# Kernel tuning notes

Measured on AMD Instinct MI355X. Metric: run time of the kernel, lower is better.

Reference implementation:

```python
import jax, jax.numpy as jnp
import numpy as np

D_MODEL = 1024
NUM_HEADS = 16
HEAD_DIM = D_MODEL // NUM_HEADS  # 64
SCALE = HEAD_DIM ** -0.5
BIAS_LEN = 128  # min(max_seq_len=512, 128)
ROPE_BASE = 10000.0
LN_EPS = 1e-5


def setup_inputs() -> dict:
    key = jax.random.key(0)
    ks = jax.random.split(key, 8)
    B, Lq, Lkv = 8, 512, 512
    return {
        "decoder_hidden": jax.random.normal(ks[0], (B, Lq, D_MODEL), jnp.float32),
        "encoder_output": jax.random.normal(ks[1], (B, Lkv, D_MODEL), jnp.float32),
        "Wqkv": jax.random.normal(ks[2], (3 * D_MODEL, D_MODEL), jnp.float32) * 0.02,
        "Wout": jax.random.normal(ks[3], (D_MODEL, D_MODEL), jnp.float32) * 0.02,
        "b_out": jnp.zeros((D_MODEL,), jnp.float32),
        "Wgate": jax.random.normal(ks[4], (D_MODEL, D_MODEL), jnp.float32) * 0.02,
        "b_gate": jnp.zeros((D_MODEL,), jnp.float32),
        "gamma": jnp.ones((D_MODEL,), jnp.float32),
        "beta": jnp.zeros((D_MODEL,), jnp.float32),
    }


def _layernorm(x, gamma, beta):
    mu = jnp.mean(x, axis=-1, keepdims=True)
    var = jnp.mean(jnp.square(x - mu), axis=-1, keepdims=True)
    return (x - mu) * jax.lax.rsqrt(var + LN_EPS) * gamma + beta


def _rope(x, cos, sin):
    # x: [B, H, L, HEAD_DIM]; cos/sin: [L, HEAD_DIM//2]
    half = HEAD_DIM // 2
    c = cos[None, None, :, :]
    s = sin[None, None, :, :]
    x_even, x_odd = x[..., :half], x[..., half:]
    return jnp.concatenate([x_even * c - x_odd * s, x_even * s + x_odd * c], axis=-1)


def _temporal_bias(L_q, L_kv):
    pos = jnp.arange(BIAS_LEN, dtype=jnp.float32)
    dist = jnp.abs(pos[None, :] - pos[:, None])  # [128,128]
    bias = jnp.exp(-dist * 0.1) - dist * 0.05
    if L_q <= BIAS_LEN and L_kv <= BIAS_LEN:
        return bias[:L_q, :L_kv]
    # bilinear interpolation (align_corners=False / half-pixel) fallback
    return jax.image.resize(bias, (L_q, L_kv), method="bilinear")


def reference(decoder_hidden, encoder_output, Wqkv, Wout, b_out, Wgate, b_gate, gamma, beta):
    B, L_q, _ = decoder_hidden.shape
    L_kv = encoder_output.shape[1]
    residual = decoder_hidden

    q_in = _layernorm(decoder_hidden, gamma, beta)
    kv_in = _layernorm(encoder_output, gamma, beta)

    q = q_in @ Wqkv[:D_MODEL].T
    k = kv_in @ Wqkv[D_MODEL:2 * D_MODEL].T
    v = kv_in @ Wqkv[2 * D_MODEL:].T

    q = q.reshape(B, L_q, NUM_HEADS, HEAD_DIM).transpose(0, 2, 1, 3)
    k = k.reshape(B, L_kv, NUM_HEADS, HEAD_DIM).transpose(0, 2, 1, 3)
    v = v.reshape(B, L_kv, NUM_HEADS, HEAD_DIM).transpose(0, 2, 1, 3)

    # rotary embedding over max(L_q, L_kv) positions
    L = max(L_q, L_kv)
    inv_freq = 1.0 / ROPE_BASE ** (jnp.arange(0, HEAD_DIM, 2, dtype=jnp.float32) / HEAD_DIM)
    freqs = jnp.arange(L, dtype=jnp.float32)[:, None] * inv_freq[None, :]  # [L, HEAD_DIM//2]
    cos, sin = jnp.cos(freqs), jnp.sin(freqs)
    q = _rope(q, cos[:L_q], sin[:L_q])
    k = _rope(k, cos[:L_kv], sin[:L_kv])

    scores = jnp.einsum("bhqd,bhkd->bhqk", q, k) * SCALE
    scores = scores + _temporal_bias(L_q, L_kv)[None, None, :, :]

    attn = jax.nn.softmax(scores, axis=-1)
    attended = jnp.einsum("bhqk,bhkd->bhqd", attn, v)
    attended = attended.transpose(0, 2, 1, 3).reshape(B, L_q, D_MODEL)
    attended = attended @ Wout.T + b_out

    gate = jax.nn.sigmoid(attended @ Wgate.T + b_gate)
    output = gate * attended + (1.0 - gate) * residual
    return output
```

## Files before the change

kernel.cpp:

```cpp
#include <hip/hip_runtime.h>
#include <hip/hip_bf16.h>

#define D_MODEL 1024
#define NHEADS 16
#define HDIM 64
#define BATCH 8
#define SEQ 512
#define NROWS 4096
#define SCALE 0.125f
#define LN_EPS 1e-5f

typedef __attribute__((ext_vector_type(8))) short bf16x8;
typedef __attribute__((ext_vector_type(4))) float f32x4;
typedef __attribute__((ext_vector_type(8))) unsigned short u16x8;

static __device__ __forceinline__ float bf2f(unsigned short u) {
    return __uint_as_float(((unsigned int)u) << 16);
}
static __device__ __forceinline__ unsigned short f2bf(float f) {
    unsigned int x = __float_as_uint(f);
    unsigned int r = (x + 0x7fffu + ((x >> 16) & 1u)) >> 16;
    return (unsigned short)r;
}

#define GLOAD16(gp, lp)                                                        \
    __builtin_amdgcn_global_load_lds(                                          \
        (const __attribute__((address_space(1))) void*)(gp),                   \
        (__attribute__((address_space(3))) void*)(lp), 16, 0, 0)

static __device__ __forceinline__ float bias128(int a, int b) {
    float d = fabsf((float)(a - b));
    return expf(-d * 0.1f) - d * 0.05f;
}

__global__ void prep_kernel(const float* __restrict__ dec, const float* __restrict__ enc,
                            const float* __restrict__ gamma, const float* __restrict__ beta,
                            const float* __restrict__ Wqkv,
                            const float* __restrict__ Wout, const float* __restrict__ Wgate,
                            unsigned short* __restrict__ q_ln, unsigned short* __restrict__ kv_ln,
                            float* __restrict__ bias, unsigned short* __restrict__ Wqkv_bf,
                            unsigned short* __restrict__ Wout_bf, unsigned short* __restrict__ Wgate_bf) {
    int blk = blockIdx.x;
    int t = threadIdx.x;
    if (blk >= 12288) {
        int idx = (blk - 12288) * 256 + t;
        const float* src; unsigned short* dst; int off;
        if (idx < 262144) { src = Wout; dst = Wout_bf; off = idx; }
        else              { src = Wgate; dst = Wgate_bf; off = idx - 262144; }
        float4 v = ((const float4*)src)[off];
        ushort4 u;
        u.x = f2bf(v.x); u.y = f2bf(v.y); u.z = f2bf(v.z); u.w = f2bf(v.w);
        ((ushort4*)dst)[off] = u;
        return;
    }
    if (blk >= 9216) {
        int idx = (blk - 9216) * 256 + t;
        float4 v = ((const float4*)Wqkv)[idx];
        ushort4 u;
        u.x = f2bf(v.x); u.y = f2bf(v.y); u.z = f2bf(v.z); u.w = f2bf(v.w);
        ((ushort4*)Wqkv_bf)[idx] = u;
        return;
    }
    if (blk >= 8192) {
        int idx = (blk - 8192) * 256 + t;
        int qi = idx >> 9, kj = idx & 511;
        float fq = (qi + 0.5f) * 0.25f - 0.5f;
        float fk = (kj + 0.5f) * 0.25f - 0.5f;
        int iq = (int)floorf(fq); float tq = fq - (float)iq;
        int ik = (int)floorf(fk); float tk = fk - (float)ik;
        int iq0 = min(max(iq, 0), 127), iq1 = min(max(iq + 1, 0), 127);
        int ik0 = min(max(ik, 0), 127), ik1 = min(max(ik + 1, 0), 127);
        float v = (1.f - tq) * ((1.f - tk) * bias128(iq0, ik0) + tk * bias128(iq0, ik1))
                +        tq  * ((1.f - tk) * bias128(iq1, ik0) + tk * bias128(iq1, ik1));
        bias[idx] = v;
        return;
    }
    int row = blk;
    const float* src = (row < NROWS) ? dec + (size_t)row * D_MODEL
                                     : enc + (size_t)(row - NROWS) * D_MODEL;
    unsigned short* dst = (row < NROWS) ? q_ln + (size_t)row * D_MODEL
                                        : kv_ln + (size_t)(row - NROWS) * D_MODEL;
    float4 x = ((const float4*)src)[t];
    float s  = x.x + x.y + x.z + x.w;
    float ss = x.x * x.x + x.y * x.y + x.z * x.z + x.w * x.w;
    #pragma unroll
    for (int off = 32; off > 0; off >>= 1) {
        s  += __shfl_down(s, off);
        ss += __shfl_down(ss, off);
    }
    __shared__ float red_s[4], red_ss[4];
    int wid = t >> 6, lane = t & 63;
    if (lane == 0) { red_s[wid] = s; red_ss[wid] = ss; }
    __syncthreads();
    if (t == 0) {
        float S = red_s[0] + red_s[1] + red_s[2] + red_s[3];
        float SS = red_ss[0] + red_ss[1] + red_ss[2] + red_ss[3];
        red_s[0] = S; red_ss[0] = SS;
    }
    __syncthreads();
    float mu  = red_s[0] * (1.0f / 1024.0f);
    float var = red_ss[0] * (1.0f / 1024.0f) - mu * mu;
    float rstd = rsqrtf(var + LN_EPS);
    float4 g = ((const float4*)gamma)[t];
    float4 bb = ((const float4*)beta)[t];
    ushort4 u;
    u.x = f2bf((x.x - mu) * rstd * g.x + bb.x);
    u.y = f2bf((x.y - mu) * rstd * g.y + bb.y);
    u.z = f2bf((x.z - mu) * rstd * g.z + bb.z);
    u.w = f2bf((x.w - mu) * rstd * g.w + bb.w);
    ((ushort4*)dst)[t] = u;
}

__global__ void convert_og(const float* __restrict__ Wout, const float* __restrict__ Wgate,
                           unsigned short* __restrict__ Wout_bf, unsigned short* __restrict__ Wgate_bf) {
    int idx = blockIdx.x * 256 + threadIdx.x;
    const float* src; unsigned short* dst; int off;
    if (idx < 262144) { src = (const float*)Wout; dst = Wout_bf; off = idx; }
    else              { src = (const float*)Wgate; dst = Wgate_bf; off = idx - 262144; }
    float4 v = ((const float4*)src)[off];
    ushort4 u;
    u.x = f2bf(v.x); u.y = f2bf(v.y); u.z = f2bf(v.z); u.w = f2bf(v.w);
    ((ushort4*)dst)[off] = u;
}

#define CSTR 136

struct alignas(16) Smem64B {
    unsigned short A[64 * 128];
    unsigned short B[128 * 128];
};

union alignas(16) Smem64Q {
    struct { unsigned short A[64 * 128]; unsigned short B[128 * 128]; } ab;
    unsigned short C[64 * CSTR];
    unsigned short Ct[128 * 72];
};

#define MF(a, b, d) __builtin_amdgcn_mfma_f32_16x16x32_bf16((a), (b), (d), 0, 0, 0)

#define GEMM_KH2B(kh)                                                          \
    {                                                                          \
        int pofs = (((kh) * 4 + quad) ^ c) * 8;                                \
        const unsigned short* Arow_ = &As2[(wr * 32 + c) * 128 + pofs];        \
        const unsigned short* Brow_ = &Bs2[(wc * 64 + c) * 128 + pofs];        \
        bf16x8 f0 = *(const bf16x8*)(Arow_);                                   \
        bf16x8 f1 = *(const bf16x8*)(Arow_ + 2048);                            \
        bf16x8 g0 = *(const bf16x8*)(Brow_);                                   \
        bf16x8 g1 = *(const bf16x8*)(Brow_ + 2048);                            \
        bf16x8 g2 = *(const bf16x8*)(Brow_ + 4096);                            \
        bf16x8 g3 = *(const bf16x8*)(Brow_ + 6144);                            \
        c00 = MF(f0, g0, c00); c01 = MF(f0, g1, c01); c02 = MF(f0, g2, c02); c03 = MF(f0, g3, c03); \
        c10 = MF(f1, g0, c10); c11 = MF(f1, g1, c11); c12 = MF(f1, g2, c12); c13 = MF(f1, g3, c13); \
    }

#define GEMM_BODY_64B(Aptr, Bptr)                                              \
    int wave = tid >> 6, lane = tid & 63, quad = lane >> 4, c = lane & 15;     \
    int wr = wave >> 1, wc = wave & 1;                                         \
    int l4 = lane >> 4, l15 = lane & 15;                                       \
    const unsigned short* Abase = (Aptr) + (size_t)(rt * 64) * 1024;           \
    const unsigned short* Bbase = (Bptr) + (size_t)(ct * 128) * 1024;          \
    int aoff0 = (wave * 16 +  0 + l4) * 1024 + ((l15 ^ ( 0 + l4)) * 8);        \
    int aoff1 = (wave * 16 +  4 + l4) * 1024 + ((l15 ^ ( 4 + l4)) * 8);        \
    int aoff2 = (wave * 16 +  8 + l4) * 1024 + ((l15 ^ ( 8 + l4)) * 8);        \
    int aoff3 = (wave * 16 + 12 + l4) * 1024 + ((l15 ^ (12 + l4)) * 8);        \
    int boff0 = (wave * 32 +  0 + l4) * 1024 + ((l15 ^ (( 0 + l4) & 15)) * 8); \
    int boff1 = (wave * 32 +  4 + l4) * 1024 + ((l15 ^ (( 4 + l4) & 15)) * 8); \
    int boff2 = (wave * 32 +  8 + l4) * 1024 + ((l15 ^ (( 8 + l4) & 15)) * 8); \
    int boff3 = (wave * 32 + 12 + l4) * 1024 + ((l15 ^ ((12 + l4) & 15)) * 8); \
    int boff4 = (wave * 32 + 16 + l4) * 1024 + ((l15 ^ ((16 + l4) & 15)) * 8); \
    int boff5 = (wave * 32 + 20 + l4) * 1024 + ((l15 ^ ((20 + l4) & 15)) * 8); \
    int boff6 = (wave * 32 + 24 + l4) * 1024 + ((l15 ^ ((24 + l4) & 15)) * 8); \
    int boff7 = (wave * 32 + 28 + l4) * 1024 + ((l15 ^ ((28 + l4) & 15)) * 8); \
    unsigned short* AsW = As2 + wave * 2048;                                   \
    unsigned short* BsW = Bs2 + wave * 4096;                                   \
    f32x4 c00 = (f32x4)0.f, c01 = (f32x4)0.f, c02 = (f32x4)0.f, c03 = (f32x4)0.f; \
    f32x4 c10 = (f32x4)0.f, c11 = (f32x4)0.f, c12 = (f32x4)0.f, c13 = (f32x4)0.f; \
    for (int kt = 0; kt < 8; ++kt) {                                           \
        int k0 = kt * 128;                                                     \
        __syncthreads();                                                       \
        GLOAD16(Abase + aoff0 + k0, AsW);                                      \
        GLOAD16(Abase + aoff1 + k0, AsW + 512);                                \
        GLOAD16(Abase + aoff2 + k0, AsW + 1024);                               \
        GLOAD16(Abase + aoff3 + k0, AsW + 1536);                               \
        GLOAD16(Bbase + boff0 + k0, BsW);                                      \
        GLOAD16(Bbase + boff1 + k0, BsW + 512);                                \
        GLOAD16(Bbase + boff2 + k0, BsW + 1024);                               \
        GLOAD16(Bbase + boff3 + k0, BsW + 1536);                               \
        GLOAD16(Bbase + boff4 + k0, BsW + 2048);                               \
        GLOAD16(Bbase + boff5 + k0, BsW + 2560);                               \
        GLOAD16(Bbase + boff6 + k0, BsW + 3072);                               \
        GLOAD16(Bbase + boff7 + k0, BsW + 3584);                               \
        __syncthreads();                                                       \
        GEMM_KH2B(0)                                                           \
        GEMM_KH2B(1)                                                           \
        GEMM_KH2B(2)                                                           \
        GEMM_KH2B(3)                                                           \
    }

#define QROPE_REG(i, reg, A0, A1, A2, A3)                                      \
    {                                                                          \
        int mloc = wr * 32 + (i) * 16 + quad * 4 + (reg);                      \
        int crow = mloc * CSTR + wc * 64;                                      \
        float fl = (float)((rt * 64 + mloc) & 511);                            \
        float aa0 = fl * inv0, aa1 = fl * inv1;                                \
        float c0 = cosf(aa0), s0 = sinf(aa0);                                  \
        float c1 = cosf(aa1), s1 = sinf(aa1);                                  \
        float e0 = A0[(reg)], o0 = A2[(reg)];                                  \
        float e1 = A1[(reg)], o1 = A3[(reg)];                                  \
        smemq.C[crow + c]      = f2bf(e0 * c0 - o0 * s0);                      \
        smemq.C[crow + 32 + c] = f2bf(e0 * s0 + o0 * c0);                      \
        smemq.C[crow + 16 + c] = f2bf(e1 * c1 - o1 * s1);                      \
        smemq.C[crow + 48 + c] = f2bf(e1 * s1 + o1 * c1);                      \
    }
#define QROPE_ROW(i, A0, A1, A2, A3)                                           \
    QROPE_REG(i, 0, A0, A1, A2, A3) QROPE_REG(i, 1, A0, A1, A2, A3)            \
    QROPE_REG(i, 2, A0, A1, A2, A3) QROPE_REG(i, 3, A0, A1, A2, A3)

#define QVSECT_REG(i, j, reg, Acc)                                             \
    smemq.Ct[(wc * 64 + (j) * 16 + c) * 72 + (wr * 32 + (i) * 16 + quad * 4 + (reg))] = f2bf(Acc[(reg)]);
#define QVSECT_TILE(i, j, Acc)                                                 \
    QVSECT_REG(i, j, 0, Acc) QVSECT_REG(i, j, 1, Acc)                          \
    QVSECT_REG(i, j, 2, Acc) QVSECT_REG(i, j, 3, Acc)

__global__ __launch_bounds__(256, 1)
void qkv_gemm_mfma(const unsigned short* __restrict__ q_ln,
                   const unsigned short* __restrict__ kv_ln,
                   const unsigned short* __restrict__ Wb,
                   unsigned short* __restrict__ qo,
                   unsigned short* __restrict__ ko,
                   unsigned short* __restrict__ vo) {
    int bid = blockIdx.x;
    int st = bid >> 5, in = bid & 31;
    int stc = st % 3, str = st / 3;
    int ct = stc * 8 + (in & 7);
    int rt = str * 4 + (in >> 3);
    int n0 = ct * 128;
    int section = n0 >> 10;
    const unsigned short* A = (section == 0) ? q_ln : kv_ln;

    __shared__ Smem64Q smemq;
    unsigned short* As2 = smemq.ab.A;
    unsigned short* Bs2 = smemq.ab.B;
    int tid = threadIdx.x;

    GEMM_BODY_64B(A, Wb)

    __syncthreads();
    if (section == 2) {
        QVSECT_TILE(0, 0, c00) QVSECT_TILE(0, 1, c01) QVSECT_TILE(0, 2, c02) QVSECT_TILE(0, 3, c03)
        QVSECT_TILE(1, 0, c10) QVSECT_TILE(1, 1, c11) QVSECT_TILE(1, 2, c12) QVSECT_TILE(1, 3, c13)
        __syncthreads();
        int dr = tid >> 1, hh = tid & 1;
        int h = ((n0 & 1023) >> 6) + (dr >> 6);
        int d = dr & 63;
        int mmb = rt * 64;
        int bb = mmb >> 9, ll0 = mmb & 511;
        unsigned short* orow = vo + (((size_t)bb * NHEADS + h) * HDIM + d) * SEQ + ll0 + hh * 32;
        const unsigned short* csrc = &smemq.Ct[dr * 72 + hh * 32];
        #pragma unroll
        for (int kc = 0; kc < 4; ++kc)
            *(u16x8*)(orow + kc * 8) = *(const u16x8*)(csrc + kc * 8);
        return;
    }

    float inv0 = expf(-0.2878231366f * (float)c);
    float inv1 = expf(-0.2878231366f * (float)(16 + c));
    QROPE_ROW(0, c00, c01, c02, c03)
    QROPE_ROW(1, c10, c11, c12, c13)
    __syncthreads();

    unsigned short* outp = (section == 0) ? qo : ko;
    int rr = tid >> 2;
    int ch = (tid >> 1) & 1;
    int sub = tid & 1;
    int mm = rt * 64 + rr;
    int bb = mm >> 9, ll = mm & 511;
    int h = ((n0 & 1023) >> 6) + ch;
    unsigned short* orow = outp + (((size_t)bb * NHEADS + h) * SEQ + ll) * HDIM + sub * 32;
    const unsigned short* csrc = &smemq.C[rr * CSTR + ch * 64 + sub * 32];
    #pragma unroll
    for (int kc = 0; kc < 4; ++kc)
        *(u16x8*)(orow + kc * 8) = *(const u16x8*)(csrc + kc * 8);
}

#define O1_REG(mb, reg, n, Acc)                                                \
    t_bf[(size_t)((mb) + (reg)) * 1024 + (n)] = f2bf(Acc[(reg)] + bo);
#define O1_TILE(i, j, Acc)                                                     \
    {                                                                          \
        int n = ct * 128 + wc * 64 + (j) * 16 + c;                             \
        float bo = b_out[n];                                                   \
        int mb = rt * 64 + wr * 32 + (i) * 16 + quad * 4;                      \
        O1_REG(mb, 0, n, Acc) O1_REG(mb, 1, n, Acc)                            \
        O1_REG(mb, 2, n, Acc) O1_REG(mb, 3, n, Acc)                            \
    }

__global__ __launch_bounds__(256, 1)
void out_gemm1_mfma(const unsigned short* __restrict__ att,
                    const unsigned short* __restrict__ Wob,
                    const float* __restrict__ b_out,
                    unsigned short* __restrict__ t_bf) {
    int ct = blockIdx.x, rt = blockIdx.y;
    __shared__ Smem64B smem2;
    unsigned short* As2 = smem2.A;
    unsigned short* Bs2 = smem2.B;
    int tid = threadIdx.x;

    GEMM_BODY_64B(att, Wob)

    O1_TILE(0, 0, c00) O1_TILE(0, 1, c01) O1_TILE(0, 2, c02) O1_TILE(0, 3, c03)
    O1_TILE(1, 0, c10) O1_TILE(1, 1, c11) O1_TILE(1, 2, c12) O1_TILE(1, 3, c13)
}

#define O2_REG(mb, reg, n, Acc)                                                \
    {                                                                          \
        float gz = Acc[(reg)] + bg;                                            \
        float g = 1.0f / (1.0f + expf(-gz));                                   \
        size_t idx = (size_t)((mb) + (reg)) * 1024 + (n);                      \
        float tv = bf2f(t_bf[idx]);                                            \
        float rv = residual[idx];                                              \
        out[idx] = g * tv + (1.0f - g) * rv;                                   \
    }
#define O2_TILE(i, j, Acc)                                                     \
    {                                                                          \
        int n = ct * 128 + wc * 64 + (j) * 16 + c;                             \
        float bg = b_gate[n];                                                  \
        int mb = rt * 64 + wr * 32 + (i) * 16 + quad * 4;                      \
        O2_REG(mb, 0, n, Acc) O2_REG(mb, 1, n, Acc)                            \
        O2_REG(mb, 2, n, Acc) O2_REG(mb, 3, n, Acc)                            \
    }

__global__ __launch_bounds__(256, 1)
void out_gemm2_mfma(const unsigned short* __restrict__ t_bf,
                    const unsigned short* __restrict__ Wgb,
                    const float* __restrict__ b_gate,
                    const float* __restrict__ residual,
                    float* __restrict__ out) {
    int ct = blockIdx.x, rt = blockIdx.y;
    __shared__ Smem64B smem2;
    unsigned short* As2 = smem2.A;
    unsigned short* Bs2 = smem2.B;
    int tid = threadIdx.x;

    GEMM_BODY_64B(t_bf, Wgb)

    O2_TILE(0, 0, c00) O2_TILE(0, 1, c01) O2_TILE(0, 2, c02) O2_TILE(0, 3, c03)
    O2_TILE(1, 0, c10) O2_TILE(1, 1, c11) O2_TILE(1, 2, c12) O2_TILE(1, 3, c13)
}

#define KSTR 72

__global__ __launch_bounds__(512)
void attn_kernel(const unsigned short* __restrict__ q,
                 const unsigned short* __restrict__ k,
                 const unsigned short* __restrict__ vt,
                 const float* __restrict__ bias,
                 unsigned short* __restrict__ attended) {
    int qt = blockIdx.x, h = blockIdx.y, b = blockIdx.z;
    __shared__ unsigned short Ks[64 * 64];
    __shared__ unsigned short Vs[64 * 64];
    __shared__ unsigned short Ps[128 * KSTR];
    __shared__ float lf[128];

    int tid = threadIdx.x;
    int wave = tid >> 6, lane = tid & 63;
    int quad = lane >> 4, c = lane & 15;
    int wb = wave * 16;
    size_t headbase = (((size_t)b * NHEADS + h) * SEQ) * HDIM;
    int q0 = qt * 128;

    const unsigned short* qrow = q + headbase + (size_t)(q0 + wb + c) * HDIM;
    bf16x8 aq0 = *(const bf16x8*)(qrow + quad * 8);
    bf16x8 aq1 = *(const bf16x8*)(qrow + 32 + quad * 8);

    int srow = wave * 8 + (lane >> 3);
    int schunk = (lane & 7) ^ (srow & 7);
    unsigned short* KsW = Ks + wave * 512;
    unsigned short* VsW = Vs + wave * 512;
    const unsigned short* kgb = k + headbase + (size_t)srow * HDIM + schunk * 8;
    const unsigned short* vgb = vt + headbase + (size_t)srow * SEQ + schunk * 8;
    int x7 = c & 7;
    int p0 = (quad ^ x7) * 8;
    int p1 = ((4 + quad) ^ x7) * 8;

    f32x4 oacc[4];
    #pragma unroll
    for (int t = 0; t < 4; ++t) oacc[t] = (f32x4)0.f;
    float lrow[4];
    #pragma unroll
    for (int r = 0; r < 4; ++r) lrow[r] = 0.f;

    for (int kt = 0; kt < 8; ++kt) {
        int kv0 = kt * 64;
        __syncthreads();
        GLOAD16(kgb + (size_t)kv0 * HDIM, KsW);
        GLOAD16(vgb + kv0, VsW);
        __syncthreads();

        f32x4 sacc[4];
        #pragma unroll
        for (int nt = 0; nt < 4; ++nt) {
            const unsigned short* kbase = &Ks[(nt * 16 + c) * 64];
            bf16x8 b0 = *(const bf16x8*)(kbase + p0);
            bf16x8 b1 = *(const bf16x8*)(kbase + p1);
            f32x4 a = (f32x4)0.f;
            a = __builtin_amdgcn_mfma_f32_16x16x32_bf16(aq0, b0, a, 0, 0, 0);
            a = __builtin_amdgcn_mfma_f32_16x16x32_bf16(aq1, b1, a, 0, 0, 0);
            sacc[nt] = a;
        }

        const float* bbase = bias + (size_t)(q0 + wb + quad * 4) * 512 + kv0 + c;
        float tsum[4];
        #pragma unroll
        for (int r = 0; r < 4; ++r) tsum[r] = 0.f;
        #pragma unroll
        for (int nt = 0; nt < 4; ++nt)
            #pragma unroll
            for (int r = 0; r < 4; ++r) {
                float p = __expf(sacc[nt][r] * SCALE + bbase[(size_t)r * 512 + nt * 16]);
                tsum[r] += p;
                Ps[(wb + quad * 4 + r) * KSTR + nt * 16 + c] = f2bf(p);
            }
        #pragma unroll
        for (int r = 0; r < 4; ++r) {
            float t = tsum[r];
            t += __shfl_xor(t, 1);
            t += __shfl_xor(t, 2);
            t += __shfl_xor(t, 4);
            t += __shfl_xor(t, 8);
            lrow[r] += t;
        }

        bf16x8 pb0 = *(const bf16x8*)&Ps[(wb + c) * KSTR + quad * 8];
        bf16x8 pb1 = *(const bf16x8*)&Ps[(wb + c) * KSTR + 32 + quad * 8];
        #pragma unroll
        for (int t = 0; t < 4; ++t) {
            const unsigned short* vbase = &Vs[(t * 16 + c) * 64];
            bf16x8 a0 = *(const bf16x8*)(vbase + p0);
            bf16x8 a1 = *(const bf16x8*)(vbase + p1);
            oacc[t] = __builtin_amdgcn_mfma_f32_16x16x32_bf16(a0, pb0, oacc[t], 0, 0, 0);
            oacc[t] = __builtin_amdgcn_mfma_f32_16x16x32_bf16(a1, pb1, oacc[t], 0, 0, 0);
        }
    }

    if (c == 0) {
        f32x4 lv;
        lv[0] = lrow[0]; lv[1] = lrow[1]; lv[2] = lrow[2]; lv[3] = lrow[3];
        *(f32x4*)&lf[wb + quad * 4] = lv;
    }
    float invl = 1.0f / lf[wb + c];
    unsigned short* drow = attended + ((size_t)b * SEQ + (q0 + wb + c)) * D_MODEL + h * HDIM;
    #pragma unroll
    for (int t = 0; t < 4; ++t) {
        ushort4 o;
        o.x = f2bf(oacc[t][0] * invl);
        o.y = f2bf(oacc[t][1] * invl);
        o.z = f2bf(oacc[t][2] * invl);
        o.w = f2bf(oacc[t][3] * invl);
        *(ushort4*)(drow + t * 16 + quad * 4) = o;
    }
}

extern "C" void kernel_launch(void* const* d_in, const int* in_sizes, int n_in,
                              void* d_out, int out_size, void* d_ws, size_t ws_size,
                              hipStream_t stream) {
    const float* dec    = (const float*)d_in[0];
    const float* enc    = (const float*)d_in[1];
    const float* Wqkv   = (const float*)d_in[2];
    const float* Wout   = (const float*)d_in[3];
    const float* b_out  = (const float*)d_in[4];
    const float* Wgate  = (const float*)d_in[5];
    const float* b_gate = (const float*)d_in[6];
    const float* gamma  = (const float*)d_in[7];
    const float* beta   = (const float*)d_in[8];
    float* out = (float*)d_out;

    char* ws = (char*)d_ws;
    const size_t MB = 1024 * 1024;
    unsigned short* q_ln    = (unsigned short*)(ws + 0 * MB);
    unsigned short* kv_ln   = (unsigned short*)(ws + 8 * MB);
    unsigned short* qb      = (unsigned short*)(ws + 16 * MB);
    unsigned short* kb      = (unsigned short*)(ws + 24 * MB);
    unsigned short* vb      = (unsigned short*)(ws + 32 * MB);
    unsigned short* Wqkv_bf = (unsigned short*)(ws + 40 * MB);
    float*          bias    = (float*)(ws + 46 * MB);
    unsigned short* att     = (unsigned short*)(ws + 0 * MB);
    unsigned short* t_bf    = (unsigned short*)(ws + 24 * MB);

    bool hoist = (ws_size >= 51 * MB);
    unsigned short* Wout_bf  = (unsigned short*)(ws + (hoist ? 47 * MB : 32 * MB));
    unsigned short* Wgate_bf = (unsigned short*)(ws + (hoist ? 49 * MB : 34 * MB));

    prep_kernel<<<hoist ? 14336 : 12288, 256, 0, stream>>>(
        dec, enc, gamma, beta, Wqkv, Wout, Wgate,
        q_ln, kv_ln, bias, Wqkv_bf, Wout_bf, Wgate_bf);
    qkv_gemm_mfma<<<1536, 256, 0, stream>>>(q_ln, kv_ln, Wqkv_bf, qb, kb, vb);
    attn_kernel<<<dim3(4, 16, 8), 512, 0, stream>>>(qb, kb, vb, bias, att);
    if (!hoist)
        convert_og<<<2048, 256, 0, stream>>>(Wout, Wgate, Wout_bf, Wgate_bf);
    out_gemm1_mfma<<<dim3(8, 64), 256, 0, stream>>>(att, Wout_bf, b_out, t_bf);
    out_gemm2_mfma<<<dim3(8, 64), 256, 0, stream>>>(t_bf, Wgate_bf, b_gate, dec, out);
}
```

Before: 210.5 us.

## Enlarge QKV GEMM tile to 128x128 with BK=64 and XCD-aware block remap

The QKV projection kernel moves from a 64x128 tile with a 128-wide K step to a 128x128 tile with a 64-wide K step, halving the grid to 768 blocks. Each wave now holds a 4x4 grid of MFMA accumulators, raising arithmetic intensity per LDS load. Block IDs are also remapped so consecutive blocks spread across the eight XCDs while neighbouring tiles share L2. The RoPE and V-transpose epilogues are rewritten for the larger tile. The cost is more accumulator registers per thread and fewer blocks, which means lower occupancy and a worse tail.

```diff
diff --git a/kernel.cpp b/kernel.cpp
--- a/kernel.cpp
+++ b/kernel.cpp
@@ -128,12 +128,6 @@
 struct alignas(16) Smem64B {
     unsigned short A[64 * 128];
     unsigned short B[128 * 128];
-};
-
-union alignas(16) Smem64Q {
-    struct { unsigned short A[64 * 128]; unsigned short B[128 * 128]; } ab;
-    unsigned short C[64 * CSTR];
-    unsigned short Ct[128 * 72];
 };
 
 #define MF(a, b, d) __builtin_amdgcn_mfma_f32_16x16x32_bf16((a), (b), (d), 0, 0, 0)
@@ -197,30 +191,10 @@
         GEMM_KH2B(3)                                                           \
     }
 
-#define QROPE_REG(i, reg, A0, A1, A2, A3)                                      \
-    {                                                                          \
-        int mloc = wr * 32 + (i) * 16 + quad * 4 + (reg);                      \
-        int crow = mloc * CSTR + wc * 64;                                      \
-        float fl = (float)((rt * 64 + mloc) & 511);                            \
-        float aa0 = fl * inv0, aa1 = fl * inv1;                                \
-        float c0 = cosf(aa0), s0 = sinf(aa0);                                  \
-        float c1 = cosf(aa1), s1 = sinf(aa1);                                  \
-        float e0 = A0[(reg)], o0 = A2[(reg)];                                  \
-        float e1 = A1[(reg)], o1 = A3[(reg)];                                  \
-        smemq.C[crow + c]      = f2bf(e0 * c0 - o0 * s0);                      \
-        smemq.C[crow + 32 + c] = f2bf(e0 * s0 + o0 * c0);                      \
-        smemq.C[crow + 16 + c] = f2bf(e1 * c1 - o1 * s1);                      \
-        smemq.C[crow + 48 + c] = f2bf(e1 * s1 + o1 * c1);                      \
-    }
-#define QROPE_ROW(i, A0, A1, A2, A3)                                           \
-    QROPE_REG(i, 0, A0, A1, A2, A3) QROPE_REG(i, 1, A0, A1, A2, A3)            \
-    QROPE_REG(i, 2, A0, A1, A2, A3) QROPE_REG(i, 3, A0, A1, A2, A3)
-
-#define QVSECT_REG(i, j, reg, Acc)                                             \
-    smemq.Ct[(wc * 64 + (j) * 16 + c) * 72 + (wr * 32 + (i) * 16 + quad * 4 + (reg))] = f2bf(Acc[(reg)]);
-#define QVSECT_TILE(i, j, Acc)                                                 \
-    QVSECT_REG(i, j, 0, Acc) QVSECT_REG(i, j, 1, Acc)                          \
-    QVSECT_REG(i, j, 2, Acc) QVSECT_REG(i, j, 3, Acc)
+union alignas(16) SmemQ2 {
+    struct { unsigned short A[128 * 64]; unsigned short B[128 * 64]; } ab;
+    unsigned short C[128 * CSTR];
+};
 
 __global__ __launch_bounds__(256, 1)
 void qkv_gemm_mfma(const unsigned short* __restrict__ q_ln,
@@ -230,56 +204,127 @@
                    unsigned short* __restrict__ ko,
                    unsigned short* __restrict__ vo) {
     int bid = blockIdx.x;
-    int st = bid >> 5, in = bid & 31;
-    int stc = st % 3, str = st / 3;
-    int ct = stc * 8 + (in & 7);
-    int rt = str * 4 + (in >> 3);
+    int wg = (bid & 7) * 96 + (bid >> 3);
+    int g = wg >> 5, idx = wg & 31;
+    int ctg = g % 3, rtg = g / 3;
+    int ct = ctg * 8 + (idx & 7);
+    int rt = rtg * 4 + (idx >> 3);
     int n0 = ct * 128;
     int section = n0 >> 10;
     const unsigned short* A = (section == 0) ? q_ln : kv_ln;
 
-    __shared__ Smem64Q smemq;
-    unsigned short* As2 = smemq.ab.A;
-    unsigned short* Bs2 = smemq.ab.B;
+    __shared__ SmemQ2 smem;
+    unsigned short* As2 = smem.ab.A;
+    unsigned short* Bs2 = smem.ab.B;
     int tid = threadIdx.x;
-
-    GEMM_BODY_64B(A, Wb)
+    int wave = tid >> 6, lane = tid & 63, quad = lane >> 4, c = lane & 15;
+    int wr = wave >> 1, wc = wave & 1;
+    int x7 = c & 7;
+
+    const unsigned short* Abase = A + (size_t)(rt * 128) * 1024;
+    const unsigned short* Bbase = Wb + (size_t)n0 * 1024;
+    int off0 = (tid >> 3) * 1024 + (((tid & 7) ^ ((tid >> 3) & 7)) * 8);
+    unsigned short* AsW = As2 + wave * 512;
+    unsigned short* BsW = Bs2 + wave * 512;
+
+    f32x4 acc[4][4];
+    #pragma unroll
+    for (int i = 0; i < 4; ++i)
+        #pragma unroll
+        for (int j = 0; j < 4; ++j) acc[i][j] = (f32x4)0.f;
+
+    for (int kt = 0; kt < 16; ++kt) {
+        int k0 = kt * 64;
+        __syncthreads();
+        GLOAD16(Abase + off0 +     0 + k0, AsW);
+        GLOAD16(Abase + off0 + 32768 + k0, AsW + 2048);
+        GLOAD16(Abase + off0 + 65536 + k0, AsW + 4096);
+        GLOAD16(Abase + off0 + 98304 + k0, AsW + 6144);
+        GLOAD16(Bbase + off0 +     0 + k0, BsW);
+        GLOAD16(Bbase + off0 + 32768 + k0, BsW + 2048);
+        GLOAD16(Bbase + off0 + 65536 + k0, BsW + 4096);
+        GLOAD16(Bbase + off0 + 98304 + k0, BsW + 6144);
+        __syncthreads();
+        #pragma unroll
+        for (int kh = 0; kh < 2; ++kh) {
+            int pofs = ((kh * 4 + quad) ^ x7) * 8;
+            const unsigned short* Ar = As2 + (wr * 64 + c) * 64 + pofs;
+            const unsigned short* Br = Bs2 + (wc * 64 + c) * 64 + pofs;
+            bf16x8 a0 = *(const bf16x8*)(Ar);
+            bf16x8 a1 = *(const bf16x8*)(Ar + 1024);
+            bf16x8 a2 = *(const bf16x8*)(Ar + 2048);
+            bf16x8 a3 = *(const bf16x8*)(Ar + 3072);
+            bf16x8 b0 = *(const bf16x8*)(Br);
+            bf16x8 b1 = *(const bf16x8*)(Br + 1024);
+            bf16x8 b2 = *(const bf16x8*)(Br + 2048);
+            bf16x8 b3 = *(const bf16x8*)(Br + 3072);
+            acc[0][0] = MF(a0, b0, acc[0][0]); acc[0][1] = MF(a0, b1, acc[0][1]);
+            acc[0][2] = MF(a0, b2, acc[0][2]); acc[0][3] = MF(a0, b3, acc[0][3]);
+            acc[1][0] = MF(a1, b0, acc[1][0]); acc[1][1] = MF(a1, b1, acc[1][1]);
+            acc[1][2] = MF(a1, b2, acc[1][2]); acc[1][3] = MF(a1, b3, acc[1][3]);
+            acc[2][0] = MF(a2, b0, acc[2][0]); acc[2][1] = MF(a2, b1, acc[2][1]);
+            acc[2][2] = MF(a2, b2, acc[2][2]); acc[2][3] = MF(a2, b3, acc[2][3]);
+            acc[3][0] = MF(a3, b0, acc[3][0]); acc[3][1] = MF(a3, b1, acc[3][1]);
+            acc[3][2] = MF(a3, b2, acc[3][2]); acc[3][3] = MF(a3, b3, acc[3][3]);
+        }
+    }
 
     __syncthreads();
+
     if (section == 2) {
-        QVSECT_TILE(0, 0, c00) QVSECT_TILE(0, 1, c01) QVSECT_TILE(0, 2, c02) QVSECT_TILE(0, 3, c03)
-        QVSECT_TILE(1, 0, c10) QVSECT_TILE(1, 1, c11) QVSECT_TILE(1, 2, c12) QVSECT_TILE(1, 3, c13)
+        #pragma unroll
+        for (int i = 0; i < 4; ++i)
+            #pragma unroll
+            for (int j = 0; j < 4; ++j)
+                #pragma unroll
+                for (int r = 0; r < 4; ++r)
+                    smem.C[(wc * 64 + j * 16 + c) * CSTR + (wr * 64 + i * 16 + quad * 4 + r)]
+                        = f2bf(acc[i][j][r]);
         __syncthreads();
         int dr = tid >> 1, hh = tid & 1;
         int h = ((n0 & 1023) >> 6) + (dr >> 6);
         int d = dr & 63;
-        int mmb = rt * 64;
-        int bb = mmb >> 9, ll0 = mmb & 511;
-        unsigned short* orow = vo + (((size_t)bb * NHEADS + h) * HDIM + d) * SEQ + ll0 + hh * 32;
-        const unsigned short* csrc = &smemq.Ct[dr * 72 + hh * 32];
-        #pragma unroll
-        for (int kc = 0; kc < 4; ++kc)
+        int m0 = rt * 128;
+        int bb = m0 >> 9, ll0 = (m0 & 511) + hh * 64;
+        unsigned short* orow = vo + (((size_t)bb * NHEADS + h) * HDIM + d) * SEQ + ll0;
+        const unsigned short* csrc = &smem.C[dr * CSTR + hh * 64];
+        #pragma unroll
+        for (int kc = 0; kc < 8; ++kc)
             *(u16x8*)(orow + kc * 8) = *(const u16x8*)(csrc + kc * 8);
         return;
     }
 
     float inv0 = expf(-0.2878231366f * (float)c);
     float inv1 = expf(-0.2878231366f * (float)(16 + c));
-    QROPE_ROW(0, c00, c01, c02, c03)
-    QROPE_ROW(1, c10, c11, c12, c13)
+    #pragma unroll
+    for (int i = 0; i < 4; ++i)
+        #pragma unroll
+        for (int r = 0; r < 4; ++r) {
+            int mloc = wr * 64 + i * 16 + quad * 4 + r;
+            float fl = (float)((rt * 128 + mloc) & 511);
+            float a0 = fl * inv0, a1 = fl * inv1;
+            float c0 = cosf(a0), s0 = sinf(a0);
+            float c1 = cosf(a1), s1 = sinf(a1);
+            float e0 = acc[i][0][r], o0 = acc[i][2][r];
+            float e1 = acc[i][1][r], o1 = acc[i][3][r];
+            int crow = mloc * CSTR + wc * 64;
+            smem.C[crow + c]      = f2bf(e0 * c0 - o0 * s0);
+            smem.C[crow + 32 + c] = f2bf(e0 * s0 + o0 * c0);
+            smem.C[crow + 16 + c] = f2bf(e1 * c1 - o1 * s1);
+            smem.C[crow + 48 + c] = f2bf(e1 * s1 + o1 * c1);
+        }
     __syncthreads();
 
     unsigned short* outp = (section == 0) ? qo : ko;
-    int rr = tid >> 2;
-    int ch = (tid >> 1) & 1;
-    int sub = tid & 1;
-    int mm = rt * 64 + rr;
+    int rr = tid >> 1;
+    int ch = tid & 1;
+    int mm = rt * 128 + rr;
     int bb = mm >> 9, ll = mm & 511;
     int h = ((n0 & 1023) >> 6) + ch;
-    unsigned short* orow = outp + (((size_t)bb * NHEADS + h) * SEQ + ll) * HDIM + sub * 32;
-    const unsigned short* csrc = &smemq.C[rr * CSTR + ch * 64 + sub * 32];
-    #pragma unroll
-    for (int kc = 0; kc < 4; ++kc)
+    unsigned short* orow = outp + (((size_t)bb * NHEADS + h) * SEQ + ll) * HDIM;
+    const unsigned short* csrc = &smem.C[rr * CSTR + ch * 64];
+    #pragma unroll
+    for (int kc = 0; kc < 8; ++kc)
         *(u16x8*)(orow + kc * 8) = *(const u16x8*)(csrc + kc * 8);
 }
 
@@ -493,7 +538,7 @@
     prep_kernel<<<hoist ? 14336 : 12288, 256, 0, stream>>>(
         dec, enc, gamma, beta, Wqkv, Wout, Wgate,
         q_ln, kv_ln, bias, Wqkv_bf, Wout_bf, Wgate_bf);
-    qkv_gemm_mfma<<<1536, 256, 0, stream>>>(q_ln, kv_ln, Wqkv_bf, qb, kb, vb);
+    qkv_gemm_mfma<<<768, 256, 0, stream>>>(q_ln, kv_ln, Wqkv_bf, qb, kb, vb);
     attn_kernel<<<dim3(4, 16, 8), 512, 0, stream>>>(qb, kb, vb, bias, att);
     if (!hoist)
         convert_og<<<2048, 256, 0, stream>>>(Wout, Wgate, Wout_bf, Wgate_bf);
```

Result: slower. 375.7 us (+78.5%).

## Double-buffer QKV GEMM K-loop and remap blocks for XCD locality

Applied to the files above, without the earlier changes.

Replaces the single-buffered 128-wide K-step GEMM body in the QKV projection kernel with a double-buffered 64-wide K pipeline, so global-to-LDS loads for the next stage are issued while MFMAs run on the current one. It also remaps block IDs so consecutive blocks dispatched to the same XCD share weight and activation tiles, aiming for better L2 reuse. The remap assumes 8 XCDs and a grid of 1536 blocks. The LDS footprint stays similar, and the K-loop now has more barriers.

```diff
diff --git a/kernel.cpp b/kernel.cpp
--- a/kernel.cpp
+++ b/kernel.cpp
@@ -128,12 +128,6 @@
 struct alignas(16) Smem64B {
     unsigned short A[64 * 128];
     unsigned short B[128 * 128];
-};
-
-union alignas(16) Smem64Q {
-    struct { unsigned short A[64 * 128]; unsigned short B[128 * 128]; } ab;
-    unsigned short C[64 * CSTR];
-    unsigned short Ct[128 * 72];
 };
 
 #define MF(a, b, d) __builtin_amdgcn_mfma_f32_16x16x32_bf16((a), (b), (d), 0, 0, 0)
@@ -197,6 +191,35 @@
         GEMM_KH2B(3)                                                           \
     }
 
+union alignas(16) SmemQD {
+    struct { unsigned short A[2][64 * 64]; unsigned short B[2][128 * 64]; } ab;
+    unsigned short C[64 * CSTR];
+    unsigned short Ct[128 * 72];
+};
+
+#define QSTAGE(pA, pB, k0)                                                     \
+    GLOAD16(Ab + (k0),          (pA) + stW);                                   \
+    GLOAD16(Ab + 32768 + (k0),  (pA) + stW + 2048);                            \
+    GLOAD16(Bb + (k0),          (pB) + stW);                                   \
+    GLOAD16(Bb + 32768 + (k0),  (pB) + stW + 2048);                            \
+    GLOAD16(Bb + 65536 + (k0),  (pB) + stW + 4096);                            \
+    GLOAD16(Bb + 98304 + (k0),  (pB) + stW + 6144);
+
+#define QKH(pA, pB, kh)                                                        \
+    {                                                                          \
+        int pofs = (((kh) * 4 + quad) ^ x7) * 8;                               \
+        const unsigned short* Ar_ = (pA) + (wr * 32 + c) * 64 + pofs;          \
+        const unsigned short* Br_ = (pB) + (wc * 64 + c) * 64 + pofs;          \
+        bf16x8 f0 = *(const bf16x8*)(Ar_);                                     \
+        bf16x8 f1 = *(const bf16x8*)(Ar_ + 1024);                              \
+        bf16x8 g0 = *(const bf16x8*)(Br_);                                     \
+        bf16x8 g1 = *(const bf16x8*)(Br_ + 1024);                              \
+        bf16x8 g2 = *(const bf16x8*)(Br_ + 2048);                              \
+        bf16x8 g3 = *(const bf16x8*)(Br_ + 3072);                              \
+        c00 = MF(f0, g0, c00); c01 = MF(f0, g1, c01); c02 = MF(f0, g2, c02); c03 = MF(f0, g3, c03); \
+        c10 = MF(f1, g0, c10); c11 = MF(f1, g1, c11); c12 = MF(f1, g2, c12); c13 = MF(f1, g3, c13); \
+    }
+
 #define QROPE_REG(i, reg, A0, A1, A2, A3)                                      \
     {                                                                          \
         int mloc = wr * 32 + (i) * 16 + quad * 4 + (reg);                      \
@@ -230,22 +253,44 @@
                    unsigned short* __restrict__ ko,
                    unsigned short* __restrict__ vo) {
     int bid = blockIdx.x;
-    int st = bid >> 5, in = bid & 31;
-    int stc = st % 3, str = st / 3;
+    int wg = (bid & 7) * 192 + (bid >> 3);
+    int st = wg >> 5, in = wg & 31;
+    int stc = st >> 4, str = st & 15;
     int ct = stc * 8 + (in & 7);
     int rt = str * 4 + (in >> 3);
     int n0 = ct * 128;
-    int section = n0 >> 10;
+    int section = stc;
     const unsigned short* A = (section == 0) ? q_ln : kv_ln;
 
-    __shared__ Smem64Q smemq;
-    unsigned short* As2 = smemq.ab.A;
-    unsigned short* Bs2 = smemq.ab.B;
+    __shared__ SmemQD smemq;
     int tid = threadIdx.x;
-
-    GEMM_BODY_64B(A, Wb)
-
+    int wave = tid >> 6, lane = tid & 63, quad = lane >> 4, c = lane & 15;
+    int wr = wave >> 1, wc = wave & 1;
+    int x7 = c & 7;
+
+    int soff = (tid >> 3) * 1024 + (((tid & 7) ^ ((tid >> 3) & 7)) * 8);
+    const unsigned short* Ab = A + (size_t)(rt * 64) * 1024 + soff;
+    const unsigned short* Bb = Wb + (size_t)n0 * 1024 + soff;
+    int stW = wave * 512;
+    unsigned short* A0 = smemq.ab.A[0];
+    unsigned short* A1 = smemq.ab.A[1];
+    unsigned short* B0 = smemq.ab.B[0];
+    unsigned short* B1 = smemq.ab.B[1];
+
+    f32x4 c00 = (f32x4)0.f, c01 = (f32x4)0.f, c02 = (f32x4)0.f, c03 = (f32x4)0.f;
+    f32x4 c10 = (f32x4)0.f, c11 = (f32x4)0.f, c12 = (f32x4)0.f, c13 = (f32x4)0.f;
+
+    QSTAGE(A0, B0, 0)
     __syncthreads();
+    for (int kt2 = 0; kt2 < 8; ++kt2) {
+        QSTAGE(A1, B1, (kt2 * 2 + 1) * 64)
+        QKH(A0, B0, 0) QKH(A0, B0, 1)
+        __syncthreads();
+        if (kt2 < 7) { QSTAGE(A0, B0, (kt2 * 2 + 2) * 64) }
+        QKH(A1, B1, 0) QKH(A1, B1, 1)
+        __syncthreads();
+    }
+
     if (section == 2) {
         QVSECT_TILE(0, 0, c00) QVSECT_TILE(0, 1, c01) QVSECT_TILE(0, 2, c02) QVSECT_TILE(0, 3, c03)
         QVSECT_TILE(1, 0, c10) QVSECT_TILE(1, 1, c11) QVSECT_TILE(1, 2, c12) QVSECT_TILE(1, 3, c13)
```

Result: no change. 208.9 us (-0.8%).
